# Kernel tuning notes

Hardware: AMD Instinct MI355X
Metric: run time of the kernel (lower is better)

The kernel has to match this reference:

```python
import jax, jax.numpy as jnp
import numpy as np

ALPHA = 0.2  # LeakyReLU negative slope
OUT_FEATURES = 64


def dsn2(t):
    # Closed-form doubly-stochastic normalization for one [N, N] slice.
    n = t.shape[0]
    rs = t.sum(axis=1, keepdims=True)          # [N, 1] row sums
    cs = t.sum(axis=0, keepdims=True)          # [1, N] col sums
    lamb = jnp.maximum(rs.max(), cs.max())
    r = n * lamb - t.sum()
    tt = t + (lamb * lamb - lamb * (rs + cs) + rs * cs) / r
    ttm = tt / tt.sum(axis=0)[0]               # divide by first column-sum (scalar), per original
    return jnp.where(t > 0, ttm, t)


def setup_inputs() -> dict:
    key = jax.random.key(0)
    k1, k2, k3, k4 = jax.random.split(key, 4)
    N, P, IN, OUT = 3072, 4, 256, OUT_FEATURES
    h = jax.random.normal(k1, (N, IN), dtype=jnp.float32)
    edge_attr = jax.random.uniform(k2, (P, N, N), dtype=jnp.float32)
    W = jax.random.normal(k3, (IN, OUT), dtype=jnp.float32) * 0.1
    a = jax.random.normal(k4, (2 * OUT, 1), dtype=jnp.float32) * 0.1
    return {"h": h, "edge_attr": edge_attr, "W": W, "a": a}


def reference(h, edge_attr, W, a):
    F = OUT_FEATURES
    Wh = h @ W                                   # [N, F]
    Wh1 = Wh @ a[:F, :]                          # [N, 1]
    Wh2 = Wh @ a[F:, :]                          # [N, 1]
    e = jax.nn.leaky_relu(Wh1 + Wh2.T, negative_slope=ALPHA)  # [N, N]
    e = e * edge_attr                            # [P, N, N]
    attention = jax.vmap(dsn2)(e)                # [P, N, N]
    h_prime = jnp.einsum('pij,jf->pif', attention, Wh)  # [P, N, F]
    # concat=True: cat along feature dim -> [N, P*F]
    N = h.shape[0]
    h_cat = jnp.transpose(h_prime, (1, 0, 2)).reshape(N, -1)
    return jax.nn.elu(h_cat), e
```

## Files before the change

kernel.cpp:

```cpp
#include <hip/hip_runtime.h>
#include <math.h>

#define NN 3072
#define PP 4
#define INF_ 256
#define FF 64
#define LEAK 0.2f
#define KB2 384
#define KS 4
#define KCH (NN / KS)
#define PNF (PP * NN * FF)

#define WH1_OFF  0
#define WH2_OFF  (WH1_OFF + NN)
#define RS_OFF   (WH2_OFF + NN)
#define CS_OFF   (RS_OFF + PP * NN)
#define U_OFF    (CS_OFF + PP * NN)
#define V_OFF    (U_OFF + PP * NN)
#define SCAL_OFF (V_OFF + PP * NN)
#define WHT_OFF  (SCAL_OFF + 8)
#define CP_OFF   (WHT_OFF + (NN * FF) / 2)

typedef short short8 __attribute__((ext_vector_type(8)));
typedef float floatx4 __attribute__((ext_vector_type(4)));

__device__ inline unsigned short f2bf(float x) {
    unsigned u = __float_as_uint(x);
    return (unsigned short)((u + 0x7FFFu + ((u >> 16) & 1u)) >> 16);
}

__global__ __launch_bounds__(64) void k1_gemm(const float* __restrict__ h,
                                              const float* __restrict__ W,
                                              const float* __restrict__ a,
                                              float* __restrict__ ws) {
    int row = blockIdx.x;
    int f = threadIdx.x;
    __shared__ float hrow[INF_];
    ((float4*)hrow)[f] = ((const float4*)(h + (size_t)row * INF_))[f];
    __syncthreads();
    float acc = 0.f;
#pragma unroll 8
    for (int k = 0; k < INF_; ++k) acc = fmaf(hrow[k], W[k * FF + f], acc);
    unsigned short* whT = (unsigned short*)(ws + WHT_OFF);
    whT[(size_t)f * NN + row] = f2bf(acc);
    float s1 = acc * a[f];
    float s2 = acc * a[FF + f];
#pragma unroll
    for (int off = 32; off > 0; off >>= 1) {
        s1 += __shfl_down(s1, off);
        s2 += __shfl_down(s2, off);
    }
    if (f == 0) { ws[WH1_OFF + row] = s1; ws[WH2_OFF + row] = s2; }
}

__global__ __launch_bounds__(256) void k2_e(const float* __restrict__ edge,
                                            float* __restrict__ e_out,
                                            float* __restrict__ ws) {
    int p = blockIdx.y;
    int row0 = blockIdx.x * 8;
    int tid = threadIdx.x;
    const float* Wh1 = ws + WH1_OFF;
    const float4* Wh2v = (const float4*)(ws + WH2_OFF);
    float4 wv[3];
#pragma unroll
    for (int c = 0; c < 3; ++c) wv[c] = Wh2v[c * 256 + tid];
    float colAcc[12];
#pragma unroll
    for (int i = 0; i < 12; ++i) colAcc[i] = 0.f;
    __shared__ float rowpart[8][4];
    const size_t slice = (size_t)p * NN * NN;
#pragma unroll 2
    for (int r = 0; r < 8; ++r) {
        int row = row0 + r;
        float w1 = Wh1[row];
        const float4* ein = (const float4*)(edge + slice + (size_t)row * NN);
        float* eoutf = e_out + slice + (size_t)row * NN;
        float racc = 0.f;
#pragma unroll
        for (int c = 0; c < 3; ++c) {
            int j4 = c * 256 + tid;
            float4 ea = ein[j4];
            float4 w = wv[c];
            floatx4 ev;
            float b;
            b = w1 + w.x; b = b > 0.f ? b : LEAK * b; ev.x = b * ea.x;
            b = w1 + w.y; b = b > 0.f ? b : LEAK * b; ev.y = b * ea.y;
            b = w1 + w.z; b = b > 0.f ? b : LEAK * b; ev.z = b * ea.z;
            b = w1 + w.w; b = b > 0.f ? b : LEAK * b; ev.w = b * ea.w;
            __builtin_nontemporal_store(ev, (floatx4*)(eoutf + (size_t)j4 * 4));
            colAcc[c * 4 + 0] += ev.x; colAcc[c * 4 + 1] += ev.y;
            colAcc[c * 4 + 2] += ev.z; colAcc[c * 4 + 3] += ev.w;
            racc += (ev.x + ev.y) + (ev.z + ev.w);
        }
#pragma unroll
        for (int off = 32; off > 0; off >>= 1) racc += __shfl_down(racc, off);
        if ((tid & 63) == 0) rowpart[r][tid >> 6] = racc;
    }
    __syncthreads();
    if (tid < 32) {
        float vv = rowpart[tid >> 2][tid & 3];
        vv += __shfl_down(vv, 2);
        vv += __shfl_down(vv, 1);
        if ((tid & 3) == 0) ws[RS_OFF + p * NN + row0 + (tid >> 2)] = vv;
    }
    float4* cp = (float4*)(ws + CP_OFF + (size_t)(p * KB2 + blockIdx.x) * NN);
#pragma unroll
    for (int c = 0; c < 3; ++c) {
        float4 cv;
        cv.x = colAcc[c * 4 + 0]; cv.y = colAcc[c * 4 + 1];
        cv.z = colAcc[c * 4 + 2]; cv.w = colAcc[c * 4 + 3];
        cp[c * 256 + tid] = cv;
    }
}

__global__ __launch_bounds__(256) void k3a_red(float* __restrict__ ws) {
    int p = blockIdx.y;
    int col = blockIdx.x * 64 + (threadIdx.x & 63);
    int chunk = threadIdx.x >> 6;
    const float* cp = ws + CP_OFF + (size_t)p * KB2 * NN + (size_t)chunk * 96 * NN + col;
    float s = 0.f;
#pragma unroll 8
    for (int b = 0; b < 96; ++b) s += cp[(size_t)b * NN];
    __shared__ float sred[4][64];
    sred[chunk][threadIdx.x & 63] = s;
    __syncthreads();
    if (threadIdx.x < 64) {
        float t = sred[0][threadIdx.x] + sred[1][threadIdx.x] +
                  sred[2][threadIdx.x] + sred[3][threadIdx.x];
        ws[CS_OFF + p * NN + col] = t;
    }
}

__global__ __launch_bounds__(256) void k3b_scal(float* __restrict__ ws) {
    int p = blockIdx.x;
    int tid = threadIdx.x;
    const float* rs = ws + RS_OFF + p * NN;
    const float* cs = ws + CS_OFF + p * NN;
    float mx = -3.4e38f, sum = 0.f;
    for (int i = tid; i < NN; i += 256) {
        float rv = rs[i], cv = cs[i];
        mx = fmaxf(mx, fmaxf(rv, cv));
        sum += rv;
    }
#pragma unroll
    for (int off = 32; off > 0; off >>= 1) {
        mx = fmaxf(mx, __shfl_down(mx, off));
        sum += __shfl_down(sum, off);
    }
    __shared__ float smx[4], ssum[4];
    __shared__ float s_lamb, s_invlr;
    if ((tid & 63) == 0) { smx[tid >> 6] = mx; ssum[tid >> 6] = sum; }
    __syncthreads();
    if (tid == 0) {
        float lamb = fmaxf(fmaxf(smx[0], smx[1]), fmaxf(smx[2], smx[3]));
        float T = ssum[0] + ssum[1] + ssum[2] + ssum[3];
        float r = (float)NN * lamb - T;
        s_lamb = lamb;
        s_invlr = 1.f / (r * lamb);
        ws[SCAL_OFF + p] = 1.f / lamb;
    }
    __syncthreads();
    float lamb = s_lamb, invlr = s_invlr;
    for (int i = tid; i < NN; i += 256) {
        ws[U_OFF + p * NN + i] = (lamb - rs[i]) * invlr;
        ws[V_OFF + p * NN + i] = lamb - cs[i];
    }
}

__global__ __launch_bounds__(64) void k4_mfma(const float* __restrict__ e_in,
                                              float* __restrict__ ws) {
    int p = blockIdx.y;
    int z = blockIdx.z;
    int row0 = blockIdx.x * 16;
    int tid = threadIdx.x;
    const unsigned short* whT = (const unsigned short*)(ws + WHT_OFF);
    const float* u = ws + U_OFF + p * NN;
    const float* v = ws + V_OFF + p * NN;
    float invl = ws[SCAL_OFF + p];
    const float* eslice = e_in + (size_t)p * NN * NN;

    const int mrow = tid & 15;
    const int kq = tid >> 4;
    float u_r = u[row0 + mrow];
    const float4* erow = (const float4*)(eslice + (size_t)(row0 + mrow) * NN);
    const float4* vrow = (const float4*)v;
    const short8* w0 = (const short8*)(whT + (size_t)(0 * 16 + mrow) * NN);
    const short8* w1 = (const short8*)(whT + (size_t)(1 * 16 + mrow) * NN);
    const short8* w2 = (const short8*)(whT + (size_t)(2 * 16 + mrow) * NN);
    const short8* w3 = (const short8*)(whT + (size_t)(3 * 16 + mrow) * NN);

    floatx4 acc[4];
#pragma unroll
    for (int nt = 0; nt < 4; ++nt)
#pragma unroll
        for (int i = 0; i < 4; ++i) acc[nt][i] = 0.f;

    const int kbase = z * KCH;
#pragma unroll 2
    for (int k0 = kbase; k0 < kbase + KCH; k0 += 32) {
        int ei = (k0 >> 2) + (kq << 1);
        float4 e0 = erow[ei];
        float4 e1 = erow[ei + 1];
        float4 v0 = vrow[ei];
        float4 v1 = vrow[ei + 1];
        int wi = (k0 >> 3) + kq;
        short8 b0 = w0[wi];
        short8 b1 = w1[wi];
        short8 b2 = w2[wi];
        short8 b3 = w3[wi];
        float a0 = e0.x > 0.f ? fmaf(u_r, v0.x, e0.x * invl) : e0.x;
        float a1 = e0.y > 0.f ? fmaf(u_r, v0.y, e0.y * invl) : e0.y;
        float a2 = e0.z > 0.f ? fmaf(u_r, v0.z, e0.z * invl) : e0.z;
        float a3 = e0.w > 0.f ? fmaf(u_r, v0.w, e0.w * invl) : e0.w;
        float a4 = e1.x > 0.f ? fmaf(u_r, v1.x, e1.x * invl) : e1.x;
        float a5 = e1.y > 0.f ? fmaf(u_r, v1.y, e1.y * invl) : e1.y;
        float a6 = e1.z > 0.f ? fmaf(u_r, v1.z, e1.z * invl) : e1.z;
        float a7 = e1.w > 0.f ? fmaf(u_r, v1.w, e1.w * invl) : e1.w;
        int4 pa;
        pa.x = (int)f2bf(a0) | ((int)f2bf(a1) << 16);
        pa.y = (int)f2bf(a2) | ((int)f2bf(a3) << 16);
        pa.z = (int)f2bf(a4) | ((int)f2bf(a5) << 16);
        pa.w = (int)f2bf(a6) | ((int)f2bf(a7) << 16);
        short8 af = *(short8*)&pa;
        acc[0] = __builtin_amdgcn_mfma_f32_16x16x32_bf16(af, b0, acc[0], 0, 0, 0);
        acc[1] = __builtin_amdgcn_mfma_f32_16x16x32_bf16(af, b1, acc[1], 0, 0, 0);
        acc[2] = __builtin_amdgcn_mfma_f32_16x16x32_bf16(af, b2, acc[2], 0, 0, 0);
        acc[3] = __builtin_amdgcn_mfma_f32_16x16x32_bf16(af, b3, acc[3], 0, 0, 0);
    }
    float* part = ws + CP_OFF + (size_t)z * PNF + (size_t)p * NN * FF + (size_t)row0 * FF;
#pragma unroll
    for (int nt = 0; nt < 4; ++nt)
#pragma unroll
        for (int r = 0; r < 4; ++r)
            part[((tid >> 4) * 4 + r) * FF + nt * 16 + (tid & 15)] = acc[nt][r];
}

__global__ __launch_bounds__(256) void k5_red(const float* __restrict__ ws,
                                              float* __restrict__ out0) {
    int i = blockIdx.x * 256 + threadIdx.x;
    const float* part = ws + CP_OFF;
    float s = part[i] + part[PNF + i] + part[2 * PNF + i] + part[3 * (size_t)PNF + i];
    s = s > 0.f ? s : (expf(s) - 1.0f);
    int f = i & 63;
    int p = i / (NN * FF);
    int n = (i - p * NN * FF) >> 6;
    out0[(size_t)n * (PP * FF) + p * FF + f] = s;
}

extern "C" void kernel_launch(void* const* d_in, const int* in_sizes, int n_in,
                              void* d_out, int out_size, void* d_ws, size_t ws_size,
                              hipStream_t stream) {
    const float* h    = (const float*)d_in[0];
    const float* edge = (const float*)d_in[1];
    const float* W    = (const float*)d_in[2];
    const float* a    = (const float*)d_in[3];
    float* out0  = (float*)d_out;
    float* e_out = out0 + (size_t)NN * PP * FF;
    float* ws = (float*)d_ws;

    k1_gemm<<<NN, 64, 0, stream>>>(h, W, a, ws);
    k2_e<<<dim3(NN / 8, PP), 256, 0, stream>>>(edge, e_out, ws);
    k3a_red<<<dim3(NN / 64, PP), 256, 0, stream>>>(ws);
    k3b_scal<<<PP, 256, 0, stream>>>(ws);
    k4_mfma<<<dim3(NN / 16, PP, KS), 64, 0, stream>>>(e_out, ws);
    k5_red<<<PNF / 256, 256, 0, stream>>>(ws, out0);
}
```

Baseline: 413.2 us.

## Stage attention GEMM tiles through swizzled shared memory with double buffering

The attention-times-Wh MFMA kernel now uses 256-thread blocks covering 32 rows. Each block cooperatively loads e, v and the bf16 WhT tile into XOR-swizzled LDS with double buffering, so four waves share the B operand instead of each wave re-reading WhT from global memory. The e-computation kernel also prefetches the next row's edge data into registers. It switches from nontemporal to ordinary stores for e, and defers the row-sum shuffles until after the loop. The cost is added LDS traffic and barriers, and the plain stores may pollute the cache.

```diff
diff --git a/kernel.cpp b/kernel.cpp
--- a/kernel.cpp
+++ b/kernel.cpp
@@ -67,31 +67,54 @@
     float colAcc[12];
 #pragma unroll
     for (int i = 0; i < 12; ++i) colAcc[i] = 0.f;
+    float racc8[8];
     __shared__ float rowpart[8][4];
     const size_t slice = (size_t)p * NN * NN;
-#pragma unroll 2
+    const float4* ein = (const float4*)(edge + slice + (size_t)row0 * NN);
+    float4* eout = (float4*)(e_out + slice + (size_t)row0 * NN);
+    float4 c0 = ein[tid], c1 = ein[256 + tid], c2 = ein[512 + tid];
+#pragma unroll
     for (int r = 0; r < 8; ++r) {
-        int row = row0 + r;
-        float w1 = Wh1[row];
-        const float4* ein = (const float4*)(edge + slice + (size_t)row * NN);
-        float* eoutf = e_out + slice + (size_t)row * NN;
+        float4 n0, n1, n2;
+        if (r < 7) {
+            const float4* nx = ein + (size_t)(r + 1) * 768;
+            n0 = nx[tid]; n1 = nx[256 + tid]; n2 = nx[512 + tid];
+        }
+        float w1 = Wh1[row0 + r];
+        float4* eor = eout + (size_t)r * 768;
         float racc = 0.f;
-#pragma unroll
-        for (int c = 0; c < 3; ++c) {
-            int j4 = c * 256 + tid;
-            float4 ea = ein[j4];
-            float4 w = wv[c];
-            floatx4 ev;
-            float b;
-            b = w1 + w.x; b = b > 0.f ? b : LEAK * b; ev.x = b * ea.x;
-            b = w1 + w.y; b = b > 0.f ? b : LEAK * b; ev.y = b * ea.y;
-            b = w1 + w.z; b = b > 0.f ? b : LEAK * b; ev.z = b * ea.z;
-            b = w1 + w.w; b = b > 0.f ? b : LEAK * b; ev.w = b * ea.w;
-            __builtin_nontemporal_store(ev, (floatx4*)(eoutf + (size_t)j4 * 4));
-            colAcc[c * 4 + 0] += ev.x; colAcc[c * 4 + 1] += ev.y;
-            colAcc[c * 4 + 2] += ev.z; colAcc[c * 4 + 3] += ev.w;
-            racc += (ev.x + ev.y) + (ev.z + ev.w);
-        }
+        float4 ea, w, ev;
+        float b;
+        ea = c0; w = wv[0];
+        b = w1 + w.x; b = b > 0.f ? b : LEAK * b; ev.x = b * ea.x;
+        b = w1 + w.y; b = b > 0.f ? b : LEAK * b; ev.y = b * ea.y;
+        b = w1 + w.z; b = b > 0.f ? b : LEAK * b; ev.z = b * ea.z;
+        b = w1 + w.w; b = b > 0.f ? b : LEAK * b; ev.w = b * ea.w;
+        eor[tid] = ev;
+        colAcc[0] += ev.x; colAcc[1] += ev.y; colAcc[2] += ev.z; colAcc[3] += ev.w;
+        racc += (ev.x + ev.y) + (ev.z + ev.w);
+        ea = c1; w = wv[1];
+        b = w1 + w.x; b = b > 0.f ? b : LEAK * b; ev.x = b * ea.x;
+        b = w1 + w.y; b = b > 0.f ? b : LEAK * b; ev.y = b * ea.y;
+        b = w1 + w.z; b = b > 0.f ? b : LEAK * b; ev.z = b * ea.z;
+        b = w1 + w.w; b = b > 0.f ? b : LEAK * b; ev.w = b * ea.w;
+        eor[256 + tid] = ev;
+        colAcc[4] += ev.x; colAcc[5] += ev.y; colAcc[6] += ev.z; colAcc[7] += ev.w;
+        racc += (ev.x + ev.y) + (ev.z + ev.w);
+        ea = c2; w = wv[2];
+        b = w1 + w.x; b = b > 0.f ? b : LEAK * b; ev.x = b * ea.x;
+        b = w1 + w.y; b = b > 0.f ? b : LEAK * b; ev.y = b * ea.y;
+        b = w1 + w.z; b = b > 0.f ? b : LEAK * b; ev.z = b * ea.z;
+        b = w1 + w.w; b = b > 0.f ? b : LEAK * b; ev.w = b * ea.w;
+        eor[512 + tid] = ev;
+        colAcc[8] += ev.x; colAcc[9] += ev.y; colAcc[10] += ev.z; colAcc[11] += ev.w;
+        racc += (ev.x + ev.y) + (ev.z + ev.w);
+        racc8[r] = racc;
+        c0 = n0; c1 = n1; c2 = n2;
+    }
+#pragma unroll
+    for (int r = 0; r < 8; ++r) {
+        float racc = racc8[r];
 #pragma unroll
         for (int off = 32; off > 0; off >>= 1) racc += __shfl_down(racc, off);
         if ((tid & 63) == 0) rowpart[r][tid >> 6] = racc;
@@ -167,72 +190,110 @@
     }
 }
 
-__global__ __launch_bounds__(64) void k4_mfma(const float* __restrict__ e_in,
-                                              float* __restrict__ ws) {
+__global__ __launch_bounds__(256) void k4_mfma(const float* __restrict__ e_in,
+                                               float* __restrict__ ws) {
     int p = blockIdx.y;
     int z = blockIdx.z;
-    int row0 = blockIdx.x * 16;
+    int row0 = blockIdx.x * 32;
     int tid = threadIdx.x;
+    int lane = tid & 63, wid = tid >> 6;
+
+    __shared__ unsigned short sA[2][32 * 64];
+    __shared__ unsigned short sB[2][64 * 64];
+
     const unsigned short* whT = (const unsigned short*)(ws + WHT_OFF);
     const float* u = ws + U_OFF + p * NN;
     const float* v = ws + V_OFF + p * NN;
     float invl = ws[SCAL_OFF + p];
     const float* eslice = e_in + (size_t)p * NN * NN;
 
-    const int mrow = tid & 15;
-    const int kq = tid >> 4;
-    float u_r = u[row0 + mrow];
-    const float4* erow = (const float4*)(eslice + (size_t)(row0 + mrow) * NN);
-    const float4* vrow = (const float4*)v;
-    const short8* w0 = (const short8*)(whT + (size_t)(0 * 16 + mrow) * NN);
-    const short8* w1 = (const short8*)(whT + (size_t)(1 * 16 + mrow) * NN);
-    const short8* w2 = (const short8*)(whT + (size_t)(2 * 16 + mrow) * NN);
-    const short8* w3 = (const short8*)(whT + (size_t)(3 * 16 + mrow) * NN);
-
-    floatx4 acc[4];
-#pragma unroll
-    for (int nt = 0; nt < 4; ++nt)
-#pragma unroll
-        for (int i = 0; i < 4; ++i) acc[nt][i] = 0.f;
+    const int ar = tid >> 3, acg = tid & 7;
+    const int bfr = tid >> 2, bkg = tid & 3;
+    const float u_r = u[row0 + ar];
+    const float* erow = eslice + (size_t)(row0 + ar) * NN;
+    const unsigned short* wrow = whT + (size_t)bfr * NN;
+    const int aswL = ((acg >> 1) ^ (ar & 7)) * 8 + (acg & 1) * 4;
+    const int aswH = (((acg >> 1) + 4) ^ (ar & 7)) * 8 + (acg & 1) * 4;
+    const int bswL = (bkg ^ (bfr & 7)) * 8;
+    const int bswH = ((bkg + 4) ^ (bfr & 7)) * 8;
+
+    const int mrow = lane & 15, kq = lane >> 4;
+    const int rt = wid & 1, ft = (wid >> 1) * 2;
+    const int arow = rt * 16 + mrow;
+    const int sw = mrow & 7;
+
+    floatx4 acc0, acc1;
+#pragma unroll
+    for (int i = 0; i < 4; ++i) { acc0[i] = 0.f; acc1[i] = 0.f; }
+
+    float4 eL, eH, vL, vH;
+    int4 bLd, bHd;
+    auto LD = [&](int k0) {
+        const float4* ep = (const float4*)(erow + k0);
+        eL = ep[acg]; eH = ep[acg + 8];
+        const float4* vp = (const float4*)(v + k0);
+        vL = vp[acg]; vH = vp[acg + 8];
+        const int4* wp = (const int4*)(wrow + k0);
+        bLd = wp[bkg]; bHd = wp[bkg + 4];
+    };
+    auto ST = [&](int b) {
+        float a0 = eL.x > 0.f ? fmaf(u_r, vL.x, eL.x * invl) : eL.x;
+        float a1 = eL.y > 0.f ? fmaf(u_r, vL.y, eL.y * invl) : eL.y;
+        float a2 = eL.z > 0.f ? fmaf(u_r, vL.z, eL.z * invl) : eL.z;
+        float a3 = eL.w > 0.f ? fmaf(u_r, vL.w, eL.w * invl) : eL.w;
+        float a4 = eH.x > 0.f ? fmaf(u_r, vH.x, eH.x * invl) : eH.x;
+        float a5 = eH.y > 0.f ? fmaf(u_r, vH.y, eH.y * invl) : eH.y;
+        float a6 = eH.z > 0.f ? fmaf(u_r, vH.z, eH.z * invl) : eH.z;
+        float a7 = eH.w > 0.f ? fmaf(u_r, vH.w, eH.w * invl) : eH.w;
+        int2 lo, hi;
+        lo.x = (int)f2bf(a0) | ((int)f2bf(a1) << 16);
+        lo.y = (int)f2bf(a2) | ((int)f2bf(a3) << 16);
+        hi.x = (int)f2bf(a4) | ((int)f2bf(a5) << 16);
+        hi.y = (int)f2bf(a6) | ((int)f2bf(a7) << 16);
+        *(int2*)&sA[b][ar * 64 + aswL] = lo;
+        *(int2*)&sA[b][ar * 64 + aswH] = hi;
+        *(int4*)&sB[b][bfr * 64 + bswL] = bLd;
+        *(int4*)&sB[b][bfr * 64 + bswH] = bHd;
+    };
+    auto MM = [&](int b) {
+        short8 a0 = *(const short8*)&sA[b][arow * 64 + (kq ^ sw) * 8];
+        short8 a1 = *(const short8*)&sA[b][arow * 64 + ((4 + kq) ^ sw) * 8];
+        int f0 = (ft * 16 + mrow) * 64;
+        int f1 = f0 + 16 * 64;
+        short8 b00 = *(const short8*)&sB[b][f0 + (kq ^ sw) * 8];
+        short8 b01 = *(const short8*)&sB[b][f0 + ((4 + kq) ^ sw) * 8];
+        short8 b10 = *(const short8*)&sB[b][f1 + (kq ^ sw) * 8];
+        short8 b11 = *(const short8*)&sB[b][f1 + ((4 + kq) ^ sw) * 8];
+        acc0 = __builtin_amdgcn_mfma_f32_16x16x32_bf16(a0, b00, acc0, 0, 0, 0);
+        acc0 = __builtin_amdgcn_mfma_f32_16x16x32_bf16(a1, b01, acc0, 0, 0, 0);
+        acc1 = __builtin_amdgcn_mfma_f32_16x16x32_bf16(a0, b10, acc1, 0, 0, 0);
+        acc1 = __builtin_amdgcn_mfma_f32_16x16x32_bf16(a1, b11, acc1, 0, 0, 0);
+    };
 
     const int kbase = z * KCH;
-#pragma unroll 2
-    for (int k0 = kbase; k0 < kbase + KCH; k0 += 32) {
-        int ei = (k0 >> 2) + (kq << 1);
-        float4 e0 = erow[ei];
-        float4 e1 = erow[ei + 1];
-        float4 v0 = vrow[ei];
-        float4 v1 = vrow[ei + 1];
-        int wi = (k0 >> 3) + kq;
-        short8 b0 = w0[wi];
-        short8 b1 = w1[wi];
-        short8 b2 = w2[wi];
-        short8 b3 = w3[wi];
-        float a0 = e0.x > 0.f ? fmaf(u_r, v0.x, e0.x * invl) : e0.x;
-        float a1 = e0.y > 0.f ? fmaf(u_r, v0.y, e0.y * invl) : e0.y;
-        float a2 = e0.z > 0.f ? fmaf(u_r, v0.z, e0.z * invl) : e0.z;
-        float a3 = e0.w > 0.f ? fmaf(u_r, v0.w, e0.w * invl) : e0.w;
-        float a4 = e1.x > 0.f ? fmaf(u_r, v1.x, e1.x * invl) : e1.x;
-        float a5 = e1.y > 0.f ? fmaf(u_r, v1.y, e1.y * invl) : e1.y;
-        float a6 = e1.z > 0.f ? fmaf(u_r, v1.z, e1.z * invl) : e1.z;
-        float a7 = e1.w > 0.f ? fmaf(u_r, v1.w, e1.w * invl) : e1.w;
-        int4 pa;
-        pa.x = (int)f2bf(a0) | ((int)f2bf(a1) << 16);
-        pa.y = (int)f2bf(a2) | ((int)f2bf(a3) << 16);
-        pa.z = (int)f2bf(a4) | ((int)f2bf(a5) << 16);
-        pa.w = (int)f2bf(a6) | ((int)f2bf(a7) << 16);
-        short8 af = *(short8*)&pa;
-        acc[0] = __builtin_amdgcn_mfma_f32_16x16x32_bf16(af, b0, acc[0], 0, 0, 0);
-        acc[1] = __builtin_amdgcn_mfma_f32_16x16x32_bf16(af, b1, acc[1], 0, 0, 0);
-        acc[2] = __builtin_amdgcn_mfma_f32_16x16x32_bf16(af, b2, acc[2], 0, 0, 0);
-        acc[3] = __builtin_amdgcn_mfma_f32_16x16x32_bf16(af, b3, acc[3], 0, 0, 0);
+    const int NSTEP = KCH / 64;
+    LD(kbase);
+    ST(0);
+    __syncthreads();
+    int buf = 0;
+    for (int step = 0; step < NSTEP; ++step) {
+        if (step + 1 < NSTEP) {
+            LD(kbase + (step + 1) * 64);
+            MM(buf);
+            ST(buf ^ 1);
+            __syncthreads();
+        } else {
+            MM(buf);
+        }
+        buf ^= 1;
     }
     float* part = ws + CP_OFF + (size_t)z * PNF + (size_t)p * NN * FF + (size_t)row0 * FF;
 #pragma unroll
-    for (int nt = 0; nt < 4; ++nt)
-#pragma unroll
-        for (int r = 0; r < 4; ++r)
-            part[((tid >> 4) * 4 + r) * FF + nt * 16 + (tid & 15)] = acc[nt][r];
+    for (int r = 0; r < 4; ++r) {
+        int crow = rt * 16 + kq * 4 + r;
+        part[crow * FF + ft * 16 + mrow] = acc0[r];
+        part[crow * FF + (ft + 1) * 16 + mrow] = acc1[r];
+    }
 }
 
 __global__ __launch_bounds__(256) void k5_red(const float* __restrict__ ws,
@@ -262,6 +323,6 @@
     k2_e<<<dim3(NN / 8, PP), 256, 0, stream>>>(edge, e_out, ws);
     k3a_red<<<dim3(NN / 64, PP), 256, 0, stream>>>(ws);
     k3b_scal<<<PP, 256, 0, stream>>>(ws);
-    k4_mfma<<<dim3(NN / 16, PP, KS), 64, 0, stream>>>(e_out, ws);
+    k4_mfma<<<dim3(NN / 32, PP, KS), 256, 0, stream>>>(e_out, ws);
     k5_red<<<PNF / 256, 256, 0, stream>>>(ws, out0);
 }
```

After: 356.4 us. -13.8%, faster.
